# Optimization experiments

Hardware: AMD Instinct MI355X
Metric: run time of the kernel (lower is better)

Reference implementation:

```python
import jax, jax.numpy as jnp
import numpy as np

E = 32        # num_local_experts
TOP_K = 4     # num_experts_per_tok
H = 1024      # hidden_size
I = 1024      # intermediate_size (expert_dim)
ALPHA = 1.702
LIMIT = 7.0
B, S = 2, 1024


def setup_inputs() -> dict:
    key = jax.random.key(0)
    ks = jax.random.split(key, 8)
    scale = 0.02
    return {
        "hidden_states": jax.random.normal(ks[0], (B, S, H), dtype=jnp.float32),
        "gate_up_proj": jax.random.normal(ks[1], (E, H, 2 * I), dtype=jnp.float32) * scale,
        "gate_up_proj_bias": jax.random.normal(ks[2], (E, 2 * I), dtype=jnp.float32) * scale,
        "down_proj": jax.random.normal(ks[3], (E, I, H), dtype=jnp.float32) * scale,
        "down_proj_bias": jax.random.normal(ks[4], (E, H), dtype=jnp.float32) * scale,
        "router_weight": jax.random.normal(ks[5], (E, H), dtype=jnp.float32) * scale,
        "router_bias": jax.random.normal(ks[6], (E,), dtype=jnp.float32) * scale,
    }


def reference(hidden_states, gate_up_proj, gate_up_proj_bias, down_proj,
              down_proj_bias, router_weight, router_bias):
    b, s, h = hidden_states.shape
    x = hidden_states.reshape(-1, h)                       # [T, H], T = B*S
    t = x.shape[0]

    # ---- router: linear -> topk -> softmax over topk -> scatter to dense scores
    router_logits = x @ router_weight.T + router_bias      # [T, E]
    top_vals, top_idx = jax.lax.top_k(router_logits, TOP_K)
    top_w = jax.nn.softmax(top_vals, axis=-1)
    router_scores = jnp.zeros_like(router_logits).at[
        jnp.arange(t)[:, None], top_idx].set(top_w)        # [T, E]

    # ---- experts (dense all-expert path, interleaved gate/up columns)
    gate_w = gate_up_proj[..., 0::2]                       # [E, H, I]
    up_w = gate_up_proj[..., 1::2]                         # [E, H, I]
    gate_b = gate_up_proj_bias[..., 0::2]                  # [E, I]
    up_b = gate_up_proj_bias[..., 1::2]                    # [E, I]

    gate = jnp.einsum('th,ehi->eti', x, gate_w) + gate_b[:, None, :]
    up = jnp.einsum('th,ehi->eti', x, up_w) + up_b[:, None, :]
    gate = jnp.minimum(gate, LIMIT)
    up = jnp.clip(up, -LIMIT, LIMIT)
    glu = gate * jax.nn.sigmoid(gate * ALPHA)
    next_states = jnp.einsum('eti,eih->eth', (up + 1.0) * glu, down_proj)
    next_states = next_states + down_proj_bias[:, None, :]  # [E, T, H]

    # ---- combine: weight each expert output by its routing score and sum
    routed = jnp.einsum('eth,te->th', next_states, router_scores)
    return routed.reshape(b, s, h), router_scores
```

## Files before the change

### kernel.cpp

```cpp
#include <hip/hip_runtime.h>
#include <cstdint>
#include <cstddef>

#define E_ 32
#define TOPK_ 4
#define H_ 1024
#define I_ 1024
#define T_ 2048
#define ALPHA_ 1.702f
#define LIMIT_ 7.0f
#define TP_ 66
#define NCH_ 32

#define NB_RTR_  2048
#define NB_CAST_ 1024
#define NB_TGUP_ 16384
#define NB_TDWN_ 8192

typedef __attribute__((ext_vector_type(8))) short s8;
typedef __attribute__((ext_vector_type(4))) float f4;

__device__ __forceinline__ unsigned short f2bf(float f) {
  unsigned int u = __float_as_uint(f);
  return (unsigned short)((u + 0x7fffu + ((u >> 16) & 1u)) >> 16);
}

__device__ __forceinline__ void gload_lds16(const unsigned short* g,
                                            unsigned short* l) {
  __builtin_amdgcn_global_load_lds(
      (const __attribute__((address_space(1))) void*)g,
      (__attribute__((address_space(3))) void*)l, 16, 0, 0);
}

__device__ __forceinline__ void transpose_body(
    const float* __restrict__ src, unsigned short* __restrict__ dst,
    int src_rows, int src_cols, int deint, int e, int c0, int r0, int tid,
    unsigned short (*ldsT)[TP_]) {
  const float* sp = src + (size_t)e * src_rows * src_cols
                        + (size_t)r0 * src_cols + c0;
  int r = tid >> 2, cq = tid & 3;
  const float* rowp = sp + (size_t)r * src_cols + cq * 4;
  #pragma unroll
  for (int j = 0; j < 4; ++j) {
    float4 v = *(const float4*)(rowp + j * 16);
    int c = cq * 4 + j * 16;
    ldsT[c + 0][r] = f2bf(v.x);
    ldsT[c + 1][r] = f2bf(v.y);
    ldsT[c + 2][r] = f2bf(v.z);
    ldsT[c + 3][r] = f2bf(v.w);
  }
  __syncthreads();
  int co = tid >> 2, hq = tid & 3;
  s8 v0 = *(s8*)&ldsT[co][hq * 16];
  s8 v1 = *(s8*)&ldsT[co][hq * 16 + 8];
  int C = c0 + co;
  size_t out_off;
  if (deint) {
    out_off = (size_t)e * src_cols * src_rows
            + (size_t)(C & 1) * (src_cols >> 1) * src_rows
            + (size_t)(C >> 1) * src_rows + r0 + hq * 16;
  } else {
    out_off = (size_t)e * src_cols * src_rows
            + (size_t)C * src_rows + r0 + hq * 16;
  }
  *(s8*)(dst + out_off) = v0;
  *(s8*)(dst + out_off + 8) = v1;
}

__global__ __launch_bounds__(256)
void prep_kernel(const float* __restrict__ x,
                 const float* __restrict__ rw,
                 const float* __restrict__ rb,
                 const float* __restrict__ gup,
                 const float* __restrict__ dwn,
                 float* __restrict__ scores,
                 int* __restrict__ counts,
                 int* __restrict__ tok_list,
                 float* __restrict__ w_list,
                 unsigned short* __restrict__ xbf,
                 unsigned short* __restrict__ wgu_b,
                 unsigned short* __restrict__ wdt_b) {
  __shared__ __align__(16) char smem[64 * TP_ * 2];
  int bid = blockIdx.x;
  int tid = threadIdx.x;

  if (bid < NB_RTR_) {
    float* partial = (float*)smem;
    float* logits  = partial + 256;
    int t = bid;
    int e = tid & 31, q = tid >> 5;
    const float4* xp = (const float4*)(x + (size_t)t * H_ + q * 128);
    const float4* wp = (const float4*)(rw + (size_t)e * H_ + q * 128);
    float s = 0.f;
    #pragma unroll 8
    for (int h = 0; h < 32; ++h) {
      float4 a = xp[h], b = wp[h];
      s += a.x * b.x + a.y * b.y + a.z * b.z + a.w * b.w;
    }
    partial[tid] = s;
    __syncthreads();
    if (tid < 32) {
      float acc = 0.f;
      #pragma unroll
      for (int j = 0; j < 8; ++j) acc += partial[j * 32 + tid];
      logits[tid] = acc + rb[tid];
    }
    __syncthreads();
    if (tid == 0) {
      float l[E_];
      #pragma unroll
      for (int i = 0; i < E_; ++i) l[i] = logits[i];
      int idx[TOPK_]; float v[TOPK_];
      for (int k = 0; k < TOPK_; ++k) {
        int bi = 0; float bv = -1e30f;
        #pragma unroll
        for (int i = 0; i < E_; ++i)
          if (l[i] > bv) { bv = l[i]; bi = i; }
        idx[k] = bi; v[k] = bv; l[bi] = -1e30f;
      }
      float m = v[0], den = 0.f, w[TOPK_];
      #pragma unroll
      for (int k = 0; k < TOPK_; ++k) { w[k] = expf(v[k] - m); den += w[k]; }
      float inv = 1.f / den;
      float* srow = scores + (size_t)t * E_;
      #pragma unroll
      for (int i = 0; i < E_; ++i) srow[i] = 0.f;
      for (int k = 0; k < TOPK_; ++k) {
        float wk = w[k] * inv;
        srow[idx[k]] = wk;
        int pos = atomicAdd(&counts[idx[k]], 1);
        tok_list[idx[k] * T_ + pos] = t * TOPK_ + k;
        w_list[idx[k] * T_ + pos] = wk;
      }
    }
  } else if (bid < NB_RTR_ + NB_CAST_) {
    int b2 = bid - NB_RTR_;
    size_t i = (size_t)(b2 * 256 + tid) * 8;
    float4 a = *(const float4*)(x + i);
    float4 b = *(const float4*)(x + i + 4);
    s8 v;
    v[0] = (short)f2bf(a.x); v[1] = (short)f2bf(a.y);
    v[2] = (short)f2bf(a.z); v[3] = (short)f2bf(a.w);
    v[4] = (short)f2bf(b.x); v[5] = (short)f2bf(b.y);
    v[6] = (short)f2bf(b.z); v[7] = (short)f2bf(b.w);
    *(s8*)(xbf + i) = v;
  } else if (bid < NB_RTR_ + NB_CAST_ + NB_TGUP_) {
    int b3 = bid - (NB_RTR_ + NB_CAST_);
    int e = b3 >> 9;
    int rem = b3 & 511;
    int c0 = (rem & 31) * 64;
    int r0 = (rem >> 5) * 64;
    transpose_body(gup, wgu_b, H_, 2 * I_, 1, e, c0, r0, tid,
                   (unsigned short (*)[TP_])smem);
  } else {
    int b4 = bid - (NB_RTR_ + NB_CAST_ + NB_TGUP_);
    int e = b4 >> 8;
    int rem = b4 & 255;
    int c0 = (rem & 15) * 64;
    int r0 = (rem >> 4) * 64;
    transpose_body(dwn, wdt_b, I_, H_, 0, e, c0, r0, tid,
                   (unsigned short (*)[TP_])smem);
  }
}

__global__ __launch_bounds__(256)
void gateup_mfma(const unsigned short* __restrict__ xb,
                 const unsigned short* __restrict__ wgu,
                 const float* __restrict__ gb,
                 const int* __restrict__ counts,
                 const int* __restrict__ tok_list,
                 unsigned short* __restrict__ act) {
  int lid = blockIdx.x;
  int xcd = lid & 7, s = lid >> 3;
  int e = (xcd << 2) + (s >> 6);
  int rem = s & 63;
  int itile = rem >> 2;
  int tb = rem & 3;

  int cnt = counts[e];
  int t0 = tb * 128;
  if (t0 >= cnt) return;
  int tid = threadIdx.x;
  int lane = tid & 63;
  int wave = tid >> 6;
  int wm = wave >> 1, wn = wave & 1;

  __shared__ __align__(16) unsigned short Xs[2][128][32];
  __shared__ __align__(16) unsigned short Wg[2][128][32];
  __shared__ int toks[128];

  if (tid < 128) {
    int slot = t0 + tid;
    toks[tid] = (slot < cnt) ? tok_list[e * T_ + slot] : -1;
  }
  __syncthreads();

  int fm = lane & 15;
  int kc = lane >> 4;
  f4 accg[4][2] = {};
  f4 accu[4][2] = {};

  int srow0 = (wave << 5) + (lane >> 2);
  int srow1 = srow0 + 16;
  int sc0 = ((lane & 3) ^ ((srow0 >> 1) & 3)) << 3;
  int sc1 = ((lane & 3) ^ ((srow1 >> 1) & 3)) << 3;
  int enc0 = toks[srow0], enc1 = toks[srow1];
  const unsigned short* srcA0 =
      xb + (size_t)((enc0 < 0) ? 0 : (enc0 >> 2)) * H_ + sc0;
  const unsigned short* srcA1 =
      xb + (size_t)((enc1 < 0) ? 0 : (enc1 >> 2)) * H_ + sc1;
  size_t R0 = (srow0 < 64) ? (size_t)(itile * 64 + srow0)
                           : (size_t)(I_ + itile * 64 + (srow0 - 64));
  size_t R1 = (srow1 < 64) ? (size_t)(itile * 64 + srow1)
                           : (size_t)(I_ + itile * 64 + (srow1 - 64));
  const unsigned short* wbase = wgu + (size_t)e * 2 * I_ * H_;
  const unsigned short* srcB0 = wbase + R0 * H_ + sc0;
  const unsigned short* srcB1 = wbase + R1 * H_ + sc1;

  int ar[4], ac[4];
  #pragma unroll
  for (int f = 0; f < 4; ++f) {
    int r = wm * 64 + f * 16 + fm;
    ar[f] = r;
    ac[f] = (kc ^ ((r >> 1) & 3)) << 3;
  }
  int brg[2], bcg[2];
  #pragma unroll
  for (int g = 0; g < 2; ++g) {
    int r = wn * 32 + g * 16 + fm;
    brg[g] = r;
    bcg[g] = (kc ^ ((r >> 1) & 3)) << 3;
  }

#define GU_ISSUE(CC, P)                                                      \
  {                                                                          \
    gload_lds16(srcA0 + (size_t)(CC) * 32, &Xs[P][(wave << 5)][0]);          \
    gload_lds16(srcA1 + (size_t)(CC) * 32, &Xs[P][(wave << 5) + 16][0]);     \
    gload_lds16(srcB0 + (size_t)(CC) * 32, &Wg[P][(wave << 5)][0]);          \
    gload_lds16(srcB1 + (size_t)(CC) * 32, &Wg[P][(wave << 5) + 16][0]);     \
  }

  GU_ISSUE(0, 0)
  GU_ISSUE(1, 1)
  asm volatile("s_waitcnt vmcnt(4)" ::: "memory");
  __builtin_amdgcn_s_barrier();
  asm volatile("" ::: "memory");

  for (int c = 0; c < NCH_; ++c) {
    int P = c & 1;
    {
      s8 a[4];
      #pragma unroll
      for (int f = 0; f < 4; ++f) a[f] = *(const s8*)&Xs[P][ar[f]][ac[f]];
      #pragma unroll
      for (int g = 0; g < 2; ++g) {
        s8 bg = *(const s8*)&Wg[P][brg[g]][bcg[g]];
        s8 bu = *(const s8*)&Wg[P][64 + brg[g]][bcg[g]];
        #pragma unroll
        for (int f = 0; f < 4; ++f) {
          accg[f][g] = __builtin_amdgcn_mfma_f32_16x16x32_bf16(a[f], bg, accg[f][g], 0, 0, 0);
          accu[f][g] = __builtin_amdgcn_mfma_f32_16x16x32_bf16(a[f], bu, accu[f][g], 0, 0, 0);
        }
      }
    }
    __builtin_amdgcn_s_barrier();
    asm volatile("" ::: "memory");
    if (c < NCH_ - 2) {
      GU_ISSUE(c + 2, P)
      asm volatile("s_waitcnt vmcnt(4)" ::: "memory");
    } else if (c == NCH_ - 2) {
      asm volatile("s_waitcnt vmcnt(0)" ::: "memory");
    }
    __builtin_amdgcn_s_barrier();
    asm volatile("" ::: "memory");
  }
#undef GU_ISSUE

  int rq = lane >> 4;
  #pragma unroll
  for (int g = 0; g < 2; ++g) {
    int i = itile * 64 + wn * 32 + g * 16 + fm;
    float bg_ = gb[e * 2 * I_ + 2 * i];
    float bu_ = gb[e * 2 * I_ + 2 * i + 1];
    #pragma unroll
    for (int f = 0; f < 4; ++f) {
      #pragma unroll
      for (int r = 0; r < 4; ++r) {
        int m = wm * 64 + f * 16 + rq * 4 + r;
        int enc = toks[m];
        if (enc < 0) continue;
        float gv = accg[f][g][r] + bg_;
        float uv = accu[f][g][r] + bu_;
        gv = fminf(gv, LIMIT_);
        uv = fminf(fmaxf(uv, -LIMIT_), LIMIT_);
        float glu = gv / (1.f + __expf(-ALPHA_ * gv));
        act[(size_t)enc * I_ + i] = f2bf((uv + 1.f) * glu);
      }
    }
  }
}

__global__ __launch_bounds__(256)
void down_mfma(const unsigned short* __restrict__ act,
               const unsigned short* __restrict__ wdt,
               const float* __restrict__ db,
               const int* __restrict__ counts,
               const int* __restrict__ tok_list,
               const float* __restrict__ w_list,
               float* __restrict__ routed) {
  int lid = blockIdx.x;
  int xcd = lid & 7, s = lid >> 3;
  int e = (xcd << 2) + (s >> 5);
  int rem = s & 31;
  int htile = rem >> 2;
  int tb = rem & 3;

  int cnt = counts[e];
  int t0 = tb * 128;
  if (t0 >= cnt) return;
  int tid = threadIdx.x;
  int lane = tid & 63;
  int wave = tid >> 6;
  int wm = wave >> 1, wn = wave & 1;

  __shared__ __align__(16) unsigned short Xs[2][128][32];
  __shared__ __align__(16) unsigned short Wd[2][128][32];
  __shared__ int toks[128];
  __shared__ float tws[128];

  if (tid < 128) {
    int slot = t0 + tid;
    bool ok = slot < cnt;
    toks[tid] = ok ? tok_list[e * T_ + slot] : -1;
    tws[tid]  = ok ? w_list[e * T_ + slot] : 0.f;
  }
  __syncthreads();

  int fm = lane & 15;
  int kc = lane >> 4;
  f4 acc[4][4] = {};

  int srow0 = (wave << 5) + (lane >> 2);
  int srow1 = srow0 + 16;
  int sc0 = ((lane & 3) ^ ((srow0 >> 1) & 3)) << 3;
  int sc1 = ((lane & 3) ^ ((srow1 >> 1) & 3)) << 3;
  int enc0 = toks[srow0], enc1 = toks[srow1];
  const unsigned short* srcA0 =
      act + (size_t)((enc0 < 0) ? 0 : enc0) * I_ + sc0;
  const unsigned short* srcA1 =
      act + (size_t)((enc1 < 0) ? 0 : enc1) * I_ + sc1;
  const unsigned short* wbase = wdt + (size_t)e * H_ * I_;
  const unsigned short* srcB0 = wbase + (size_t)(htile * 128 + srow0) * I_ + sc0;
  const unsigned short* srcB1 = wbase + (size_t)(htile * 128 + srow1) * I_ + sc1;

  int ar[4], ac_[4];
  #pragma unroll
  for (int f = 0; f < 4; ++f) {
    int r = wm * 64 + f * 16 + fm;
    ar[f] = r;
    ac_[f] = (kc ^ ((r >> 1) & 3)) << 3;
  }
  int brg[4], bcg[4];
  #pragma unroll
  for (int g = 0; g < 4; ++g) {
    int r = wn * 64 + g * 16 + fm;
    brg[g] = r;
    bcg[g] = (kc ^ ((r >> 1) & 3)) << 3;
  }

#define DN_ISSUE(CC, P)                                                      \
  {                                                                          \
    gload_lds16(srcA0 + (size_t)(CC) * 32, &Xs[P][(wave << 5)][0]);          \
    gload_lds16(srcA1 + (size_t)(CC) * 32, &Xs[P][(wave << 5) + 16][0]);     \
    gload_lds16(srcB0 + (size_t)(CC) * 32, &Wd[P][(wave << 5)][0]);          \
    gload_lds16(srcB1 + (size_t)(CC) * 32, &Wd[P][(wave << 5) + 16][0]);     \
  }

  DN_ISSUE(0, 0)
  DN_ISSUE(1, 1)
  asm volatile("s_waitcnt vmcnt(4)" ::: "memory");
  __builtin_amdgcn_s_barrier();
  asm volatile("" ::: "memory");

  for (int c = 0; c < NCH_; ++c) {
    int P = c & 1;
    {
      s8 a[4];
      #pragma unroll
      for (int f = 0; f < 4; ++f) a[f] = *(const s8*)&Xs[P][ar[f]][ac_[f]];
      #pragma unroll
      for (int g = 0; g < 4; ++g) {
        s8 b = *(const s8*)&Wd[P][brg[g]][bcg[g]];
        #pragma unroll
        for (int f = 0; f < 4; ++f)
          acc[f][g] = __builtin_amdgcn_mfma_f32_16x16x32_bf16(a[f], b, acc[f][g], 0, 0, 0);
      }
    }
    __builtin_amdgcn_s_barrier();
    asm volatile("" ::: "memory");
    if (c < NCH_ - 2) {
      DN_ISSUE(c + 2, P)
      asm volatile("s_waitcnt vmcnt(4)" ::: "memory");
    } else if (c == NCH_ - 2) {
      asm volatile("s_waitcnt vmcnt(0)" ::: "memory");
    }
    __builtin_amdgcn_s_barrier();
    asm volatile("" ::: "memory");
  }
#undef DN_ISSUE

  int rq = lane >> 4;
  #pragma unroll
  for (int g = 0; g < 4; ++g) {
    int h = htile * 128 + wn * 64 + g * 16 + fm;
    float bias = db[e * H_ + h];
    #pragma unroll
    for (int f = 0; f < 4; ++f) {
      #pragma unroll
      for (int r = 0; r < 4; ++r) {
        int m = wm * 64 + f * 16 + rq * 4 + r;
        int enc = toks[m];
        if (enc < 0) continue;
        atomicAdd(&routed[(size_t)(enc >> 2) * H_ + h],
                  (acc[f][g][r] + bias) * tws[m]);
      }
    }
  }
}

extern "C" void kernel_launch(void* const* d_in, const int* in_sizes, int n_in,
                              void* d_out, int out_size, void* d_ws, size_t ws_size,
                              hipStream_t stream) {
  (void)in_sizes; (void)n_in; (void)out_size; (void)ws_size;
  const float* x    = (const float*)d_in[0];
  const float* gup  = (const float*)d_in[1];
  const float* gupb = (const float*)d_in[2];
  const float* dwn  = (const float*)d_in[3];
  const float* dwnb = (const float*)d_in[4];
  const float* rw   = (const float*)d_in[5];
  const float* rb   = (const float*)d_in[6];

  float* routed = (float*)d_out;
  float* scores = (float*)d_out + (size_t)T_ * H_;

  char* ws = (char*)d_ws;
  int*   counts   = (int*)ws;
  int*   tok_list = (int*)(ws + ((size_t)1 << 20));
  float* w_list   = (float*)(ws + ((size_t)1 << 20) + (size_t)E_ * T_ * 4);
  unsigned short* xbf = (unsigned short*)(ws + ((size_t)2 << 20));
  unsigned short* act = (unsigned short*)(ws + ((size_t)8 << 20));
  unsigned short* wgu_b = (unsigned short*)(ws + ((size_t)24 << 20));
  unsigned short* wdt_b = (unsigned short*)(ws + ((size_t)24 << 20)
                                            + (size_t)E_ * 2 * I_ * H_ * 2);

  hipMemsetAsync(counts, 0, E_ * sizeof(int), stream);
  hipMemsetAsync(routed, 0, (size_t)T_ * H_ * sizeof(float), stream);

  prep_kernel<<<NB_RTR_ + NB_CAST_ + NB_TGUP_ + NB_TDWN_, 256, 0, stream>>>(
      x, rw, rb, gup, dwn, scores, counts, tok_list, w_list, xbf, wgu_b, wdt_b);
  gateup_mfma<<<2048, 256, 0, stream>>>(xbf, wgu_b, gupb, counts, tok_list, act);
  down_mfma<<<1024, 256, 0, stream>>>(act, wdt_b, dwnb, counts, tok_list,
                                      w_list, routed);
}
```

Before: 751.5 us.

## Enlarge weight transpose tiles and fold output zeroing into prep kernel

Rewrites the fp32→bf16 weight transpose so each block handles a 256x128 tile, with each thread packing eight rows into 16-byte LDS and global stores, instead of a 64x64 tile with scalar LDS writes. This cuts the block count eightfold and widens the stores, reducing per-block overhead and LDS store traffic. The separate memset of the routed output is replaced by extra zeroing blocks inside the prep kernel, saving one launch. The larger LDS footprint (about 66 KB) lowers occupancy for every block in the prep kernel, including the router blocks.

```diff
diff --git a/kernel.cpp b/kernel.cpp
--- a/kernel.cpp
+++ b/kernel.cpp
@@ -9,13 +9,13 @@
 #define T_ 2048
 #define ALPHA_ 1.702f
 #define LIMIT_ 7.0f
-#define TP_ 66
 #define NCH_ 32
 
 #define NB_RTR_  2048
 #define NB_CAST_ 1024
-#define NB_TGUP_ 16384
-#define NB_TDWN_ 8192
+#define NB_TGUP_ 2048
+#define NB_TDWN_ 1024
+#define NB_ZERO_ 2048
 
 typedef __attribute__((ext_vector_type(8))) short s8;
 typedef __attribute__((ext_vector_type(4))) float f4;
@@ -32,39 +32,60 @@
       (__attribute__((address_space(3))) void*)l, 16, 0, 0);
 }
 
-__device__ __forceinline__ void transpose_body(
+__device__ __forceinline__ void transpose_body2(
     const float* __restrict__ src, unsigned short* __restrict__ dst,
-    int src_rows, int src_cols, int deint, int e, int c0, int r0, int tid,
-    unsigned short (*ldsT)[TP_]) {
+    int src_rows, int src_cols, int deint, int e, int kbase, int cbase,
+    int tid, unsigned short (*ldsT)[264]) {
+  int l = tid & 63, w = tid >> 6;
   const float* sp = src + (size_t)e * src_rows * src_cols
-                        + (size_t)r0 * src_cols + c0;
-  int r = tid >> 2, cq = tid & 3;
-  const float* rowp = sp + (size_t)r * src_cols + cq * 4;
-  #pragma unroll
-  for (int j = 0; j < 4; ++j) {
-    float4 v = *(const float4*)(rowp + j * 16);
-    int c = cq * 4 + j * 16;
-    ldsT[c + 0][r] = f2bf(v.x);
-    ldsT[c + 1][r] = f2bf(v.y);
-    ldsT[c + 2][r] = f2bf(v.z);
-    ldsT[c + 3][r] = f2bf(v.w);
+                  + (size_t)kbase * src_cols + cbase;
+  int halfw = l >> 5;
+  int m = l & 31;
+  int c4 = m * 4;
+  int n0, n1, n2, n3;
+  if (deint) { n0 = m * 2; n1 = 64 + m * 2; n2 = m * 2 + 1; n3 = 65 + m * 2; }
+  else       { n0 = c4; n1 = c4 + 1; n2 = c4 + 2; n3 = c4 + 3; }
+  int rgrp = (w * 2 + halfw) * 8;
+
+  #pragma unroll
+  for (int o = 0; o < 4; ++o) {
+    int krow = o * 64 + rgrp;
+    s8 a0, a1, a2, a3;
+    #pragma unroll
+    for (int s = 0; s < 8; ++s) {
+      float4 v = *(const float4*)(sp + (size_t)(krow + s) * src_cols + c4);
+      a0[s] = (short)f2bf(v.x);
+      a1[s] = (short)f2bf(v.y);
+      a2[s] = (short)f2bf(v.z);
+      a3[s] = (short)f2bf(v.w);
+    }
+    *(s8*)&ldsT[n0][krow] = a0;
+    *(s8*)&ldsT[n1][krow] = a1;
+    *(s8*)&ldsT[n2][krow] = a2;
+    *(s8*)&ldsT[n3][krow] = a3;
   }
   __syncthreads();
-  int co = tid >> 2, hq = tid & 3;
-  s8 v0 = *(s8*)&ldsT[co][hq * 16];
-  s8 v1 = *(s8*)&ldsT[co][hq * 16 + 8];
-  int C = c0 + co;
-  size_t out_off;
-  if (deint) {
-    out_off = (size_t)e * src_cols * src_rows
-            + (size_t)(C & 1) * (src_cols >> 1) * src_rows
-            + (size_t)(C >> 1) * src_rows + r0 + hq * 16;
-  } else {
-    out_off = (size_t)e * src_cols * src_rows
-            + (size_t)C * src_rows + r0 + hq * 16;
-  }
-  *(s8*)(dst + out_off) = v0;
-  *(s8*)(dst + out_off + 8) = v1;
+
+  int kc = m * 8;
+  int cw = w * 2 + halfw;
+  #pragma unroll
+  for (int s = 0; s < 16; ++s) {
+    int n = cw + s * 8;
+    s8 v = *(const s8*)&ldsT[n][kc];
+    size_t off;
+    if (deint) {
+      size_t plane = (n >= 64) ? 1 : 0;
+      size_t i = (size_t)(cbase >> 1) + (n & 63);
+      off = (size_t)e * src_cols * src_rows
+          + plane * (size_t)(src_cols >> 1) * src_rows
+          + i * src_rows + kbase + kc;
+    } else {
+      off = (size_t)e * src_cols * src_rows
+          + (size_t)(cbase + n) * src_rows + kbase + kc;
+    }
+    *(s8*)(dst + off) = v;
+  }
+  __syncthreads();
 }
 
 __global__ __launch_bounds__(256)
@@ -79,13 +100,14 @@
                  float* __restrict__ w_list,
                  unsigned short* __restrict__ xbf,
                  unsigned short* __restrict__ wgu_b,
-                 unsigned short* __restrict__ wdt_b) {
-  __shared__ __align__(16) char smem[64 * TP_ * 2];
+                 unsigned short* __restrict__ wdt_b,
+                 float* __restrict__ routed) {
+  __shared__ __align__(16) unsigned short ldsT[128][264];
   int bid = blockIdx.x;
   int tid = threadIdx.x;
 
   if (bid < NB_RTR_) {
-    float* partial = (float*)smem;
+    float* partial = (float*)ldsT;
     float* logits  = partial + 256;
     int t = bid;
     int e = tid & 31, q = tid >> 5;
@@ -146,20 +168,22 @@
     *(s8*)(xbf + i) = v;
   } else if (bid < NB_RTR_ + NB_CAST_ + NB_TGUP_) {
     int b3 = bid - (NB_RTR_ + NB_CAST_);
-    int e = b3 >> 9;
-    int rem = b3 & 511;
-    int c0 = (rem & 31) * 64;
-    int r0 = (rem >> 5) * 64;
-    transpose_body(gup, wgu_b, H_, 2 * I_, 1, e, c0, r0, tid,
-                   (unsigned short (*)[TP_])smem);
+    int e = b3 >> 6;
+    int rem = b3 & 63;
+    int kbase = (rem >> 4) * 256;
+    int cbase = (rem & 15) * 128;
+    transpose_body2(gup, wgu_b, H_, 2 * I_, 1, e, kbase, cbase, tid, ldsT);
+  } else if (bid < NB_RTR_ + NB_CAST_ + NB_TGUP_ + NB_TDWN_) {
+    int b4 = bid - (NB_RTR_ + NB_CAST_ + NB_TGUP_);
+    int e = b4 >> 5;
+    int rem = b4 & 31;
+    int kbase = (rem >> 3) * 256;
+    int cbase = (rem & 7) * 128;
+    transpose_body2(dwn, wdt_b, I_, H_, 0, e, kbase, cbase, tid, ldsT);
   } else {
-    int b4 = bid - (NB_RTR_ + NB_CAST_ + NB_TGUP_);
-    int e = b4 >> 8;
-    int rem = b4 & 255;
-    int c0 = (rem & 15) * 64;
-    int r0 = (rem >> 4) * 64;
-    transpose_body(dwn, wdt_b, I_, H_, 0, e, c0, r0, tid,
-                   (unsigned short (*)[TP_])smem);
+    int b5 = bid - (NB_RTR_ + NB_CAST_ + NB_TGUP_ + NB_TDWN_);
+    float4 z = {0.f, 0.f, 0.f, 0.f};
+    *(float4*)(routed + (size_t)b5 * 1024 + tid * 4) = z;
   }
 }
 
@@ -454,10 +478,10 @@
                                             + (size_t)E_ * 2 * I_ * H_ * 2);
 
   hipMemsetAsync(counts, 0, E_ * sizeof(int), stream);
-  hipMemsetAsync(routed, 0, (size_t)T_ * H_ * sizeof(float), stream);
-
-  prep_kernel<<<NB_RTR_ + NB_CAST_ + NB_TGUP_ + NB_TDWN_, 256, 0, stream>>>(
-      x, rw, rb, gup, dwn, scores, counts, tok_list, w_list, xbf, wgu_b, wdt_b);
+
+  prep_kernel<<<NB_RTR_ + NB_CAST_ + NB_TGUP_ + NB_TDWN_ + NB_ZERO_, 256, 0,
+                stream>>>(x, rw, rb, gup, dwn, scores, counts, tok_list,
+                          w_list, xbf, wgu_b, wdt_b, routed);
   gateup_mfma<<<2048, 256, 0, stream>>>(xbf, wgu_b, gupb, counts, tok_list, act);
   down_mfma<<<1024, 256, 0, stream>>>(act, wdt_b, dwnb, counts, tok_list,
                                       w_list, routed);
```

New measurement: 740.3 us. No clear change (-1.5%).
